# Kernel tuning notes

Hardware: AMD Instinct MI355X
Metric: run time of the kernel (lower is better)

The kernel has to match this reference:

```python
import jax, jax.numpy as jnp
import numpy as np

N_EVENTS = 16
N_SAMPLES = 2 ** 15          # 32768
STEP = 256                   # window_size // 2
LONG_WINDOW = 4096
LONG_COEFFS = LONG_WINDOW // 2 + 1   # 2049
LONG_STEP = LONG_WINDOW // 2         # 2048
LONG_FRAMES = N_SAMPLES // LONG_STEP # 16
N_FRAMES = N_SAMPLES // STEP         # 128
B = 8                                 # audio batch
BE = B * N_EVENTS                     # event batch = 128


def setup_inputs() -> dict:
    key = jax.random.key(0)
    k1, k2, k3, k4 = jax.random.split(key, 4)
    env = jax.random.uniform(k1, (BE, LONG_WINDOW, LONG_FRAMES), jnp.float32)
    tf = jax.random.normal(k2, (BE, LONG_COEFFS * 2, LONG_FRAMES), jnp.float32)
    noise = jax.random.uniform(k3, (BE, LONG_WINDOW, LONG_FRAMES), jnp.float32)
    indices = jax.random.randint(k4, (B, N_EVENTS), 0, N_FRAMES, dtype=jnp.int32)
    return {"env": env, "tf": tf, "noise": noise, "indices": indices}


def _event_render(env, tf, noise):
    # env, noise: (BE, LONG_WINDOW, LONG_FRAMES); tf: (BE, 2*LONG_COEFFS, LONG_FRAMES)
    batch = env.shape[0]
    energy = env * (noise * 2.0 - 1.0)  # uniform_(-1, 1) noise scaled by amp

    # magnitude = norm over interleaved (real, imag) pairs, per torch view semantics
    pairs = tf.reshape(batch, LONG_COEFFS, 2, LONG_FRAMES)
    mag = jnp.sqrt(jnp.sum(pairs * pairs, axis=2))  # (batch, C, F)
    mx = jnp.max(mag.reshape(batch, -1), axis=-1, keepdims=True)
    mag = (mag.reshape(batch, -1) / (mx + 1e-8)).reshape(batch, LONG_COEFFS, LONG_FRAMES)
    imag = tf[:, LONG_COEFFS:, :]
    phase = jnp.arctan2(imag, mag) * np.pi  # torch.angle(complex(mag, imag)) * pi
    tfc = mag * jnp.exp(1j * phase)         # complex transfer fn (batch, C, F)

    # sequential per-frame recurrence: state feeds through rfft/irfft filtering
    e_t = jnp.transpose(energy, (2, 0, 1))  # (F, batch, W)
    t_t = jnp.transpose(tfc, (2, 0, 1))     # (F, batch, C)

    def step(prev, inp):
        e, t = inp
        local = prev + e
        spec = jnp.fft.rfft(local, axis=-1, norm='ortho') * t
        frame = jnp.fft.irfft(spec, n=LONG_WINDOW, axis=-1, norm='ortho')
        return frame, frame

    init = jnp.zeros((batch, LONG_WINDOW), energy.dtype)
    _, frames = jax.lax.scan(step, init, (e_t, t_t))   # (F, batch, W)
    frames = jnp.transpose(frames, (1, 0, 2))          # (batch, F, W)

    # overlap-add with hop = LONG_STEP = W/2: split frames into halves and add
    halves = frames.reshape(batch, LONG_FRAMES, 2, LONG_STEP)
    out = jnp.zeros((batch, LONG_FRAMES + 1, LONG_STEP), frames.dtype)
    out = out.at[:, :LONG_FRAMES].add(halves[:, :, 0])
    out = out.at[:, 1:].add(halves[:, :, 1])
    return out.reshape(batch, -1)[:, :N_SAMPLES]       # (BE, N_SAMPLES)


def _segment_render(atoms, indices):
    # atoms: (BE, N_SAMPLES) -> (B, N_EVENTS, N_SAMPLES); scatter-add at time offsets
    x = atoms.reshape(B, N_EVENTS, N_SAMPLES)
    times = indices * STEP                                      # (B, E)
    pos = times[:, :, None] + jnp.arange(N_SAMPLES)[None, None, :]  # (B, E, S)
    out = jnp.zeros((B, 2 * N_SAMPLES), x.dtype)
    bidx = jnp.arange(B)[:, None, None]
    out = out.at[bidx, pos].add(x)
    return out[:, None, :N_SAMPLES]                             # (B, 1, N_SAMPLES)


def reference(env, tf, noise, indices):
    atoms = _event_render(env, tf, noise)
    return _segment_render(atoms, indices)
```

## Files before the change

### kernel.cpp

```cpp
#include <hip/hip_runtime.h>
#include <math.h>

#define TWO_PI 6.283185307179586f

#define OFF_ET   0ull
#define OFF_E    8388608ull
#define OFF_MAXP 16781312ull
#define OFF_Z    16782336ull

__device__ __forceinline__ int sw2(int n) { return n ^ ((n >> 4) & 15); }

__device__ __forceinline__ int permf(int k) {
    return ((k & 1) << 10) | (((k >> 1) & 3) << 8) | (((k >> 3) & 3) << 6)
         | (((k >> 5) & 3) << 4) | (((k >> 7) & 3) << 2) | ((k >> 9) & 3);
}

__device__ __forceinline__ void r4f_core(float2* b, int p0, int p1, int p2, int p3,
                                         float c1, float s1, float c2, float s2, float c3, float s3) {
    float2 A = b[p0], Bv = b[p1], C = b[p2], D = b[p3];
    float u0r = A.x + C.x, u0i = A.y + C.y;
    float u1r = A.x - C.x, u1i = A.y - C.y;
    float u2r = Bv.x + D.x, u2i = Bv.y + D.y;
    float u3r = Bv.x - D.x, u3i = Bv.y - D.y;
    b[p0] = make_float2(u0r + u2r, u0i + u2i);
    float z1r = u1r + u3i, z1i = u1i - u3r;
    b[p1] = make_float2(z1r * c1 + z1i * s1, z1i * c1 - z1r * s1);
    float z2r = u0r - u2r, z2i = u0i - u2i;
    b[p2] = make_float2(z2r * c2 + z2i * s2, z2i * c2 - z2r * s2);
    float z3r = u1r - u3i, z3i = u1i + u3r;
    b[p3] = make_float2(z3r * c3 + z3i * s3, z3i * c3 - z3r * s3);
}

__device__ __forceinline__ void r4i_core(float2* b, int p0, int p1, int p2, int p3,
                                         float c1, float s1, float c2, float s2, float c3, float s3) {
    float2 z0 = b[p0], z1 = b[p1], z2 = b[p2], z3 = b[p3];
    float t1r = z1.x * c1 - z1.y * s1, t1i = z1.y * c1 + z1.x * s1;
    float t2r = z2.x * c2 - z2.y * s2, t2i = z2.y * c2 + z2.x * s2;
    float t3r = z3.x * c3 - z3.y * s3, t3i = z3.y * c3 + z3.x * s3;
    float u0r = z0.x + t2r, u0i = z0.y + t2i;
    float u1r = z0.x - t2r, u1i = z0.y - t2i;
    float u2r = t1r + t3r, u2i = t1i + t3i;
    float u3r = t1r - t3r, u3i = t1i - t3i;
    b[p0] = make_float2(u0r + u2r, u0i + u2i);
    b[p1] = make_float2(u1r - u3i, u1i + u3r);
    b[p2] = make_float2(u0r - u2r, u0i - u2i);
    b[p3] = make_float2(u1r + u3i, u1i - u3r);
}

#define STAGE4X(CORE, JEXPR, H, ANGEXPR)                                       \
    {                                                                          \
        _Pragma("unroll")                                                      \
        for (int half_ = 0; half_ < 2; ++half_) {                              \
            int b_ = tid + half_ * 1024;                                       \
            int i_ = b_ & 511;                                                 \
            float2* bb_ = B2 + (b_ >> 9) * 2048;                               \
            int j_ = (JEXPR);                                                  \
            int p0 = sw2(j_), p1 = sw2(j_ + (H)), p2 = sw2(j_ + 2 * (H)),      \
                p3 = sw2(j_ + 3 * (H));                                        \
            float s1, c1; __sincosf((ANGEXPR), &s1, &c1);                      \
            float c2 = c1 * c1 - s1 * s1, s2 = 2.f * c1 * s1;                  \
            float c3 = c1 * c2 - s1 * s2, s3 = s1 * c2 + c1 * s2;              \
            CORE(bb_, p0, p1, p2, p3, c1, s1, c2, s2, c3, s3);                 \
        }                                                                      \
    }                                                                          \
    __syncthreads();

__global__ __launch_bounds__(1024, 8) void k_fwd(const float* __restrict__ env,
                                                 const float* __restrict__ noise,
                                                 const float* __restrict__ tf,
                                                 float* __restrict__ ws) {
    __shared__ float2 B2[8192];
    int tid = threadIdx.x;
    int id = blockIdx.x;
    int xcd = id & 7, slot = id >> 3;
    int be = xcd * 16 + (slot >> 2);
    int fg = slot & 3;
    const float4* env4 = (const float4*)env;
    const float4* noi4 = (const float4*)noise;
    size_t base = (size_t)be * 16384 + fg;

#pragma unroll
    for (int it = 0; it < 2; ++it) {
        int c = tid + it * 1024;
        float4 ea = env4[base + (size_t)(2 * c) * 4];
        float4 eb = env4[base + (size_t)(2 * c + 1) * 4];
        float4 za = noi4[base + (size_t)(2 * c) * 4];
        float4 zb = noi4[base + (size_t)(2 * c + 1) * 4];
        int m = sw2(c);
        B2[m]        = make_float2(ea.x * (za.x * 2.f - 1.f), eb.x * (zb.x * 2.f - 1.f));
        B2[2048 + m] = make_float2(ea.y * (za.y * 2.f - 1.f), eb.y * (zb.y * 2.f - 1.f));
        B2[4096 + m] = make_float2(ea.z * (za.z * 2.f - 1.f), eb.z * (zb.z * 2.f - 1.f));
        B2[6144 + m] = make_float2(ea.w * (za.w * 2.f - 1.f), eb.w * (zb.w * 2.f - 1.f));
    }
    __syncthreads();
    {
        int i = tid;
        int sj = sw2(i), sjb = sw2(i + 1024);
        float s, c; __sincosf((float)i * (TWO_PI / 2048.0f), &s, &c);
#pragma unroll
        for (int j4 = 0; j4 < 4; ++j4) {
            float2* bb = B2 + j4 * 2048;
            float2 a = bb[sj], b = bb[sjb];
            float dr = a.x - b.x, di = a.y - b.y;
            bb[sj] = make_float2(a.x + b.x, a.y + b.y);
            bb[sjb] = make_float2(dr * c + di * s, di * c - dr * s);
        }
    }
    __syncthreads();
    STAGE4X(r4f_core, (i_ >> 8) * 1024 + (i_ & 255), 256, (float)(i_ & 255) * (TWO_PI / 1024.0f));
    STAGE4X(r4f_core, (i_ >> 6) * 256 + (i_ & 63), 64, (float)(i_ & 63) * (TWO_PI / 256.0f));
    STAGE4X(r4f_core, (i_ >> 4) * 64 + (i_ & 15), 16, (float)(i_ & 15) * (TWO_PI / 64.0f));
    STAGE4X(r4f_core, (i_ >> 2) * 16 + (i_ & 3), 4, (float)(i_ & 3) * (TWO_PI / 16.0f));
    STAGE4X(r4f_core, i_ * 4, 1, 0.0f);
    float2* Ebase = (float2*)(ws + OFF_E) + (size_t)(be * 16 + fg * 4) * 2049;
    for (int k = tid; k <= 1024; k += 1024) {
        int pk = sw2(permf(k));
        int pm = sw2(permf((2048 - k) & 2047));
        float s4, c4; __sincosf((float)k * (TWO_PI / 4096.0f), &s4, &c4);
#pragma unroll
        for (int j4 = 0; j4 < 4; ++j4) {
            float2* bb = B2 + j4 * 2048;
            float2 zk = bb[pk], zm = bb[pm];
            float xer = 0.5f * (zk.x + zm.x), xei = 0.5f * (zk.y - zm.y);
            float xor_ = 0.5f * (zk.y + zm.y), xoi = 0.5f * (zm.x - zk.x);
            float wr = xor_ * c4 + xoi * s4;
            float wi = xoi * c4 - xor_ * s4;
            float2* Eg = Ebase + (size_t)j4 * 2049;
            Eg[k] = make_float2(xer + wr, xei + wi);
            Eg[2048 - k] = make_float2(xer - wr, wi - xei);
        }
    }
    __syncthreads();
    float* Bf = (float*)B2;
    const float4* ab4 = (const float4*)(tf + (size_t)be * 65568);
    int b0 = fg * 513;
    int nb = (fg == 3) ? 510 : 513;
    float mx = 0.f;
    for (int u = tid; u < nb * 4; u += 1024) {
        int g = u >> 2, e = u & 3;
        int bin = b0 + g;
        float4 A = ab4[bin * 8 + e];
        float4 Bv = ab4[bin * 8 + e + 4];
        mx = fmaxf(mx, fmaxf(fmaxf(A.x * A.x + Bv.x * Bv.x, A.y * A.y + Bv.y * Bv.y),
                             fmaxf(A.z * A.z + Bv.z * Bv.z, A.w * A.w + Bv.w * Bv.w)));
    }
    Bf[tid] = mx;
    __syncthreads();
    for (int s = 512; s > 0; s >>= 1) {
        if (tid < s) Bf[tid] = fmaxf(Bf[tid], Bf[tid + s]);
        __syncthreads();
    }
    if (tid == 0) ws[OFF_MAXP + be * 4 + fg] = Bf[0];
}

__global__ __launch_bounds__(256) void k_recur(const float* __restrict__ tf,
                                               float* __restrict__ ws) {
    __shared__ float sm2lo[256 * 17], simlo[256 * 17];
    __shared__ float sm2hi[256 * 17], simhi[256 * 17];
    int tid = threadIdx.x;
    int be = blockIdx.y;
    int k0 = blockIdx.x << 8;
    int hi0 = 1793 - k0;
    const float* tfb = tf + (size_t)be * 65568;
    const float4* ab4 = (const float4*)tfb;
    const float4* im4 = (const float4*)(tfb + 32784);

    for (int u = tid; u < 2048; u += 256) {
        int half = u >> 10, v = u & 1023;
        int g = v >> 2, e = v & 3;
        int bin = half ? (hi0 + g) : (k0 + g);
        float4 A = ab4[bin * 8 + e];
        float4 Bv = ab4[bin * 8 + e + 4];
        float4 I = im4[bin * 4 + e];
        int o = g * 17 + e * 4;
        float* sm = half ? sm2hi : sm2lo;
        float* si = half ? simhi : simlo;
        sm[o + 0] = A.x * A.x + Bv.x * Bv.x;
        sm[o + 1] = A.y * A.y + Bv.y * Bv.y;
        sm[o + 2] = A.z * A.z + Bv.z * Bv.z;
        sm[o + 3] = A.w * A.w + Bv.w * Bv.w;
        si[o + 0] = I.x; si[o + 1] = I.y; si[o + 2] = I.z; si[o + 3] = I.w;
    }
    __syncthreads();

    int k = k0 + tid;
    int m = 2048 - k;
    int rhi = 255 - tid;
    const float* mp = ws + OFF_MAXP + be * 4;
    float m2x = fmaxf(fmaxf(mp[0], mp[1]), fmaxf(mp[2], mp[3]));
    float rden = 1.0f / (sqrtf(m2x) + 1e-8f);
    const float2* Eb = (const float2*)(ws + OFF_E) + (size_t)be * 16 * 2049;
    float2* Zb = (float2*)(ws + OFF_Z) + (size_t)be * 16 * 2048;
    float2 evlo[16], evhi[16];
#pragma unroll
    for (int f = 0; f < 16; ++f) {
        evlo[f] = Eb[(size_t)f * 2049 + k];
        evhi[f] = Eb[(size_t)f * 2049 + m];
    }
    float ym = (k == 0) ? 0.0f : 1.0f;
    float s4, c4; __sincosf((float)k * (TWO_PI / 4096.0f), &s4, &c4);
    const float SCL = 1.0f / 2048.0f;
    float srl = 0.f, sil = 0.f, srh = 0.f, sih = 0.f;
#pragma unroll
    for (int f = 0; f < 16; ++f) {
        float mh = sqrtf(sm2lo[tid * 17 + f]) * rden;
        float ph = atan2f(simlo[tid * 17 + f], mh) * 3.14159265358979f;
        float sp, cp; __sincosf(ph, &sp, &cp);
        float Tr = mh * cp, Ti = mh * sp;
        sil *= ym;
        srl += evlo[f].x; sil += evlo[f].y;
        float nr = srl * Tr - sil * Ti;
        sil = srl * Ti + sil * Tr; srl = nr;
        float mh2 = sqrtf(sm2hi[rhi * 17 + f]) * rden;
        float ph2 = atan2f(simhi[rhi * 17 + f], mh2) * 3.14159265358979f;
        float sp2, cp2; __sincosf(ph2, &sp2, &cp2);
        float Tr2 = mh2 * cp2, Ti2 = mh2 * sp2;
        sih *= ym;
        srh += evhi[f].x; sih += evhi[f].y;
        float nr2 = srh * Tr2 - sih * Ti2;
        sih = srh * Ti2 + sih * Tr2; srh = nr2;
        float2* Zf = Zb + (size_t)f * 2048;
        if (k == 0) {
            float y0 = srl * SCL, yn = srh * SCL;
            Zf[0] = make_float2(0.5f * (y0 + yn), 0.5f * (y0 - yn));
        } else {
            float ykr = srl * SCL, yki = sil * SCL;
            float ymr = srh * SCL, ymi = sih * SCL;
            float er = 0.5f * (ykr + ymr), ei = 0.5f * (yki - ymi);
            float dr = ykr - ymr, di = yki + ymi;
            float orr = 0.5f * (dr * c4 - di * s4);
            float oi = 0.5f * (dr * s4 + di * c4);
            Zf[k] = make_float2(er - oi, ei + orr);
            Zf[m] = make_float2(er + oi, orr - ei);
        }
    }
    if (k0 == 0 && tid == 0) {
        float sr = 0.f, si = 0.f;
#pragma unroll
        for (int f = 0; f < 16; ++f) {
            float a = tfb[1024 * 32 + f];
            float b = tfb[1024 * 32 + 16 + f];
            float im = tfb[32784 + 1024 * 16 + f];
            float mh = sqrtf(a * a + b * b) * rden;
            float ph = atan2f(im, mh) * 3.14159265358979f;
            float sp, cp; __sincosf(ph, &sp, &cp);
            float Tr = mh * cp, Ti = mh * sp;
            float2 e = Eb[(size_t)f * 2049 + 1024];
            sr += e.x; si += e.y;
            float nr = sr * Tr - si * Ti;
            si = sr * Ti + si * Tr; sr = nr;
            Zb[(size_t)f * 2048 + 1024] = make_float2(sr * SCL, -si * SCL);
        }
    }
}

__global__ __launch_bounds__(1024, 8) void k_fft_inv(float* __restrict__ ws) {
    __shared__ float2 B2[8192];
    int tid = threadIdx.x;
    int be = blockIdx.x >> 2, fg = blockIdx.x & 3;
    const float2* Zbase = (const float2*)(ws + OFF_Z) + (size_t)(be * 16 + fg * 4) * 2048;
    float4 v[4];
#pragma unroll
    for (int j4 = 0; j4 < 4; ++j4)
        v[j4] = ((const float4*)(Zbase + (size_t)j4 * 2048))[tid];
    {
        int n0 = tid * 2;
        int p0 = sw2(permf(n0)), p1 = sw2(permf(n0 + 1));
#pragma unroll
        for (int j4 = 0; j4 < 4; ++j4) {
            float2* bb = B2 + j4 * 2048;
            bb[p0] = make_float2(v[j4].x, v[j4].y);
            bb[p1] = make_float2(v[j4].z, v[j4].w);
        }
    }
    __syncthreads();
    STAGE4X(r4i_core, i_ * 4, 1, 0.0f);
    STAGE4X(r4i_core, (i_ >> 2) * 16 + (i_ & 3), 4, (float)(i_ & 3) * (TWO_PI / 16.0f));
    STAGE4X(r4i_core, (i_ >> 4) * 64 + (i_ & 15), 16, (float)(i_ & 15) * (TWO_PI / 64.0f));
    STAGE4X(r4i_core, (i_ >> 6) * 256 + (i_ & 63), 64, (float)(i_ & 63) * (TWO_PI / 256.0f));
    STAGE4X(r4i_core, (i_ >> 8) * 1024 + (i_ & 255), 256, (float)(i_ & 255) * (TWO_PI / 1024.0f));
    {
        int i = tid;
        int sj = sw2(i), sjb = sw2(i + 1024);
        float s, c; __sincosf((float)i * (TWO_PI / 2048.0f), &s, &c);
#pragma unroll
        for (int j4 = 0; j4 < 4; ++j4) {
            float2* bb = B2 + j4 * 2048;
            float2 b = bb[sjb];
            float tr = b.x * c - b.y * s, ti2 = b.x * s + b.y * c;
            float2 a = bb[sj];
            bb[sj] = make_float2(a.x + tr, a.y + ti2);
            bb[sjb] = make_float2(a.x - tr, a.y - ti2);
        }
    }
    __syncthreads();
    float2* Fbase = (float2*)(ws + OFF_ET) + (size_t)(be * 16 + fg * 4) * 2048;
#pragma unroll
    for (int j4 = 0; j4 < 4; ++j4) {
        float2* bb = B2 + j4 * 2048;
        float2* Fg = Fbase + (size_t)j4 * 2048;
#pragma unroll
        for (int it = 0; it < 2; ++it) {
            int m = tid + it * 1024;
            Fg[m] = bb[sw2(m)];
        }
    }
}

__global__ __launch_bounds__(256) void k_segment(const float* __restrict__ ws,
                                                 const int* __restrict__ indices,
                                                 float* __restrict__ out) {
    __shared__ int ste[16];
    int tid = threadIdx.x;
    int b = blockIdx.y;
    if (tid < 16) ste[tid] = indices[b * 16 + tid] * 256;
    __syncthreads();
    int g = blockIdx.x * 256 + tid;
    int t = g << 2;
    const float* F = ws + OFF_ET;
    float4 acc = make_float4(0.f, 0.f, 0.f, 0.f);
#pragma unroll
    for (int e = 0; e < 16; ++e) {
        int te = ste[e];
        if (t >= te) {
            int d = t - te;
            int j = d >> 11, r = d & 2047;
            size_t base = (size_t)(b * 16 + e) * 65536;
            float4 v = *(const float4*)(F + base + j * 4096 + r);
            acc.x += v.x; acc.y += v.y; acc.z += v.z; acc.w += v.w;
            if (j >= 1) {
                float4 w = *(const float4*)(F + base + (j - 1) * 4096 + 2048 + r);
                acc.x += w.x; acc.y += w.y; acc.z += w.z; acc.w += w.w;
            }
        }
    }
    ((float4*)out)[(size_t)b * 8192 + g] = acc;
}

extern "C" void kernel_launch(void* const* d_in, const int* in_sizes, int n_in,
                              void* d_out, int out_size, void* d_ws, size_t ws_size,
                              hipStream_t stream) {
    const float* env = (const float*)d_in[0];
    const float* tf = (const float*)d_in[1];
    const float* noise = (const float*)d_in[2];
    const int* indices = (const int*)d_in[3];
    float* ws = (float*)d_ws;
    float* out = (float*)d_out;

    k_fwd<<<dim3(512), dim3(1024), 0, stream>>>(env, noise, tf, ws);
    k_recur<<<dim3(4, 128), dim3(256), 0, stream>>>(tf, ws);
    k_fft_inv<<<dim3(512), dim3(1024), 0, stream>>>(ws);
    k_segment<<<dim3(32, 8), dim3(256), 0, stream>>>(ws, indices, out);
}
```

Baseline: 88.72 us.

## Replace radix-2/4 FFT stages with radix-8 passes and fewer barriers

Rewrites the 2048-point complex FFTs in the forward and inverse kernels as three radix-8 stages plus one radix-4 stage, in place of one radix-2 and five radix-4 stages. Each group of 256 threads now owns one of the four buffers, and a new 5-bit XOR swizzle with a matching digit-reversal permutation replaces the old ones. The goal is fewer shared-memory passes and __syncthreads barriers, plus fewer twiddle sincos calls. In exchange each thread holds more registers, and twiddles are built by repeated complex multiplication, which may cost some accuracy.

```diff
diff --git a/kernel.cpp b/kernel.cpp
--- a/kernel.cpp
+++ b/kernel.cpp
@@ -8,62 +8,103 @@
 #define OFF_MAXP 16781312ull
 #define OFF_Z    16782336ull
 
-__device__ __forceinline__ int sw2(int n) { return n ^ ((n >> 4) & 15); }
-
-__device__ __forceinline__ int permf(int k) {
-    return ((k & 1) << 10) | (((k >> 1) & 3) << 8) | (((k >> 3) & 3) << 6)
-         | (((k >> 5) & 3) << 4) | (((k >> 7) & 3) << 2) | ((k >> 9) & 3);
-}
-
-__device__ __forceinline__ void r4f_core(float2* b, int p0, int p1, int p2, int p3,
-                                         float c1, float s1, float c2, float s2, float c3, float s3) {
-    float2 A = b[p0], Bv = b[p1], C = b[p2], D = b[p3];
-    float u0r = A.x + C.x, u0i = A.y + C.y;
-    float u1r = A.x - C.x, u1i = A.y - C.y;
-    float u2r = Bv.x + D.x, u2i = Bv.y + D.y;
-    float u3r = Bv.x - D.x, u3i = Bv.y - D.y;
-    b[p0] = make_float2(u0r + u2r, u0i + u2i);
-    float z1r = u1r + u3i, z1i = u1i - u3r;
-    b[p1] = make_float2(z1r * c1 + z1i * s1, z1i * c1 - z1r * s1);
-    float z2r = u0r - u2r, z2i = u0i - u2i;
-    b[p2] = make_float2(z2r * c2 + z2i * s2, z2i * c2 - z2r * s2);
-    float z3r = u1r - u3i, z3i = u1i + u3r;
-    b[p3] = make_float2(z3r * c3 + z3i * s3, z3i * c3 - z3r * s3);
-}
-
-__device__ __forceinline__ void r4i_core(float2* b, int p0, int p1, int p2, int p3,
-                                         float c1, float s1, float c2, float s2, float c3, float s3) {
-    float2 z0 = b[p0], z1 = b[p1], z2 = b[p2], z3 = b[p3];
-    float t1r = z1.x * c1 - z1.y * s1, t1i = z1.y * c1 + z1.x * s1;
-    float t2r = z2.x * c2 - z2.y * s2, t2i = z2.y * c2 + z2.x * s2;
-    float t3r = z3.x * c3 - z3.y * s3, t3i = z3.y * c3 + z3.x * s3;
-    float u0r = z0.x + t2r, u0i = z0.y + t2i;
-    float u1r = z0.x - t2r, u1i = z0.y - t2i;
-    float u2r = t1r + t3r, u2i = t1i + t3i;
-    float u3r = t1r - t3r, u3i = t1i - t3i;
-    b[p0] = make_float2(u0r + u2r, u0i + u2i);
-    b[p1] = make_float2(u1r - u3i, u1i + u3r);
-    b[p2] = make_float2(u0r - u2r, u0i - u2i);
-    b[p3] = make_float2(u1r + u3i, u1i - u3r);
-}
-
-#define STAGE4X(CORE, JEXPR, H, ANGEXPR)                                       \
-    {                                                                          \
-        _Pragma("unroll")                                                      \
-        for (int half_ = 0; half_ < 2; ++half_) {                              \
-            int b_ = tid + half_ * 1024;                                       \
-            int i_ = b_ & 511;                                                 \
-            float2* bb_ = B2 + (b_ >> 9) * 2048;                               \
-            int j_ = (JEXPR);                                                  \
-            int p0 = sw2(j_), p1 = sw2(j_ + (H)), p2 = sw2(j_ + 2 * (H)),      \
-                p3 = sw2(j_ + 3 * (H));                                        \
-            float s1, c1; __sincosf((ANGEXPR), &s1, &c1);                      \
-            float c2 = c1 * c1 - s1 * s1, s2 = 2.f * c1 * s1;                  \
-            float c3 = c1 * c2 - s1 * s2, s3 = s1 * c2 + c1 * s2;              \
-            CORE(bb_, p0, p1, p2, p3, c1, s1, c2, s2, c3, s3);                 \
-        }                                                                      \
-    }                                                                          \
-    __syncthreads();
+__device__ __forceinline__ int sw(int i) { return i ^ ((i >> 5) & 31); }
+
+__device__ __forceinline__ int posf(int k) {
+    return ((k & 7) << 8) | (((k >> 3) & 7) << 5) | (((k >> 6) & 7) << 2) | (k >> 9);
+}
+
+__device__ __forceinline__ float2 cmul(float2 a, float2 b) {
+    return make_float2(a.x * b.x - a.y * b.y, a.x * b.y + a.y * b.x);
+}
+__device__ __forceinline__ float2 cadd(float2 a, float2 b) { return make_float2(a.x + b.x, a.y + b.y); }
+__device__ __forceinline__ float2 csub(float2 a, float2 b) { return make_float2(a.x - b.x, a.y - b.y); }
+
+#define RH 0.70710678118654752f
+
+__device__ __forceinline__ void r8f(float2* b, int i0, int stride, float theta) {
+    float2 x0 = b[sw(i0)],            x1 = b[sw(i0 + stride)];
+    float2 x2 = b[sw(i0 + 2*stride)], x3 = b[sw(i0 + 3*stride)];
+    float2 x4 = b[sw(i0 + 4*stride)], x5 = b[sw(i0 + 5*stride)];
+    float2 x6 = b[sw(i0 + 6*stride)], x7 = b[sw(i0 + 7*stride)];
+    float2 t0 = cadd(x0, x4), t1 = csub(x0, x4), t2 = cadd(x2, x6), t3 = csub(x2, x6);
+    float2 A0 = cadd(t0, t2), A2 = csub(t0, t2);
+    float2 A1 = make_float2(t1.x + t3.y, t1.y - t3.x);
+    float2 A3 = make_float2(t1.x - t3.y, t1.y + t3.x);
+    float2 u0 = cadd(x1, x5), u1 = csub(x1, x5), u2 = cadd(x3, x7), u3 = csub(x3, x7);
+    float2 B0 = cadd(u0, u2), B2 = csub(u0, u2);
+    float2 B1 = make_float2(u1.x + u3.y, u1.y - u3.x);
+    float2 B3 = make_float2(u1.x - u3.y, u1.y + u3.x);
+    float2 b1 = make_float2((B1.x + B1.y) * RH, (B1.y - B1.x) * RH);
+    float2 b2 = make_float2(B2.y, -B2.x);
+    float2 b3 = make_float2((B3.y - B3.x) * RH, -(B3.x + B3.y) * RH);
+    float2 y0 = cadd(A0, B0), y4 = csub(A0, B0);
+    float2 y1 = cadd(A1, b1), y5 = csub(A1, b1);
+    float2 y2 = cadd(A2, b2), y6 = csub(A2, b2);
+    float2 y3 = cadd(A3, b3), y7 = csub(A3, b3);
+    float s1, c1; __sincosf(theta, &s1, &c1);
+    float2 w1 = make_float2(c1, -s1), w = w1;
+    y1 = cmul(y1, w); w = cmul(w, w1);
+    y2 = cmul(y2, w); w = cmul(w, w1);
+    y3 = cmul(y3, w); w = cmul(w, w1);
+    y4 = cmul(y4, w); w = cmul(w, w1);
+    y5 = cmul(y5, w); w = cmul(w, w1);
+    y6 = cmul(y6, w); w = cmul(w, w1);
+    y7 = cmul(y7, w);
+    b[sw(i0)]            = y0; b[sw(i0 + stride)]   = y1;
+    b[sw(i0 + 2*stride)] = y2; b[sw(i0 + 3*stride)] = y3;
+    b[sw(i0 + 4*stride)] = y4; b[sw(i0 + 5*stride)] = y5;
+    b[sw(i0 + 6*stride)] = y6; b[sw(i0 + 7*stride)] = y7;
+}
+
+__device__ __forceinline__ void r4f(float2* b, int i0) {
+    float2 a0 = b[sw(i0)], a1 = b[sw(i0 + 1)], a2 = b[sw(i0 + 2)], a3 = b[sw(i0 + 3)];
+    float2 t0 = cadd(a0, a2), t1 = csub(a0, a2), t2 = cadd(a1, a3), t3 = csub(a1, a3);
+    b[sw(i0)]     = cadd(t0, t2);
+    b[sw(i0 + 1)] = make_float2(t1.x + t3.y, t1.y - t3.x);
+    b[sw(i0 + 2)] = csub(t0, t2);
+    b[sw(i0 + 3)] = make_float2(t1.x - t3.y, t1.y + t3.x);
+}
+
+__device__ __forceinline__ void r8i(float2* b, int i0, int stride, float theta) {
+    float2 z0 = b[sw(i0)],            z1 = b[sw(i0 + stride)];
+    float2 z2 = b[sw(i0 + 2*stride)], z3 = b[sw(i0 + 3*stride)];
+    float2 z4 = b[sw(i0 + 4*stride)], z5 = b[sw(i0 + 5*stride)];
+    float2 z6 = b[sw(i0 + 6*stride)], z7 = b[sw(i0 + 7*stride)];
+    float s1, c1; __sincosf(theta, &s1, &c1);
+    float2 w1 = make_float2(c1, s1), w = w1;
+    z1 = cmul(z1, w); w = cmul(w, w1);
+    z2 = cmul(z2, w); w = cmul(w, w1);
+    z3 = cmul(z3, w); w = cmul(w, w1);
+    z4 = cmul(z4, w); w = cmul(w, w1);
+    z5 = cmul(z5, w); w = cmul(w, w1);
+    z6 = cmul(z6, w); w = cmul(w, w1);
+    z7 = cmul(z7, w);
+    float2 t0 = cadd(z0, z4), t1 = csub(z0, z4), t2 = cadd(z2, z6), t3 = csub(z2, z6);
+    float2 A0 = cadd(t0, t2), A2 = csub(t0, t2);
+    float2 A1 = make_float2(t1.x - t3.y, t1.y + t3.x);
+    float2 A3 = make_float2(t1.x + t3.y, t1.y - t3.x);
+    float2 u0 = cadd(z1, z5), u1 = csub(z1, z5), u2 = cadd(z3, z7), u3 = csub(z3, z7);
+    float2 B0 = cadd(u0, u2), B2 = csub(u0, u2);
+    float2 B1 = make_float2(u1.x - u3.y, u1.y + u3.x);
+    float2 B3 = make_float2(u1.x + u3.y, u1.y - u3.x);
+    float2 b1 = make_float2((B1.x - B1.y) * RH, (B1.x + B1.y) * RH);
+    float2 b2 = make_float2(-B2.y, B2.x);
+    float2 b3 = make_float2(-(B3.x + B3.y) * RH, (B3.x - B3.y) * RH);
+    b[sw(i0)]            = cadd(A0, B0); b[sw(i0 + 4*stride)] = csub(A0, B0);
+    b[sw(i0 + stride)]   = cadd(A1, b1); b[sw(i0 + 5*stride)] = csub(A1, b1);
+    b[sw(i0 + 2*stride)] = cadd(A2, b2); b[sw(i0 + 6*stride)] = csub(A2, b2);
+    b[sw(i0 + 3*stride)] = cadd(A3, b3); b[sw(i0 + 7*stride)] = csub(A3, b3);
+}
+
+__device__ __forceinline__ void r4i(float2* b, int i0) {
+    float2 a0 = b[sw(i0)], a1 = b[sw(i0 + 1)], a2 = b[sw(i0 + 2)], a3 = b[sw(i0 + 3)];
+    float2 t0 = cadd(a0, a2), t1 = csub(a0, a2), t2 = cadd(a1, a3), t3 = csub(a1, a3);
+    b[sw(i0)]     = cadd(t0, t2);
+    b[sw(i0 + 1)] = make_float2(t1.x - t3.y, t1.y + t3.x);
+    b[sw(i0 + 2)] = csub(t0, t2);
+    b[sw(i0 + 3)] = make_float2(t1.x + t3.y, t1.y - t3.x);
+}
 
 __global__ __launch_bounds__(1024, 8) void k_fwd(const float* __restrict__ env,
                                                  const float* __restrict__ noise,
@@ -78,7 +119,6 @@
     const float4* env4 = (const float4*)env;
     const float4* noi4 = (const float4*)noise;
     size_t base = (size_t)be * 16384 + fg;
-
 #pragma unroll
     for (int it = 0; it < 2; ++it) {
         int c = tid + it * 1024;
@@ -86,46 +126,36 @@
         float4 eb = env4[base + (size_t)(2 * c + 1) * 4];
         float4 za = noi4[base + (size_t)(2 * c) * 4];
         float4 zb = noi4[base + (size_t)(2 * c + 1) * 4];
-        int m = sw2(c);
+        int m = sw(c);
         B2[m]        = make_float2(ea.x * (za.x * 2.f - 1.f), eb.x * (zb.x * 2.f - 1.f));
         B2[2048 + m] = make_float2(ea.y * (za.y * 2.f - 1.f), eb.y * (zb.y * 2.f - 1.f));
         B2[4096 + m] = make_float2(ea.z * (za.z * 2.f - 1.f), eb.z * (zb.z * 2.f - 1.f));
         B2[6144 + m] = make_float2(ea.w * (za.w * 2.f - 1.f), eb.w * (zb.w * 2.f - 1.f));
     }
     __syncthreads();
-    {
-        int i = tid;
-        int sj = sw2(i), sjb = sw2(i + 1024);
-        float s, c; __sincosf((float)i * (TWO_PI / 2048.0f), &s, &c);
-#pragma unroll
-        for (int j4 = 0; j4 < 4; ++j4) {
-            float2* bb = B2 + j4 * 2048;
-            float2 a = bb[sj], b = bb[sjb];
-            float dr = a.x - b.x, di = a.y - b.y;
-            bb[sj] = make_float2(a.x + b.x, a.y + b.y);
-            bb[sjb] = make_float2(dr * c + di * s, di * c - dr * s);
-        }
-    }
-    __syncthreads();
-    STAGE4X(r4f_core, (i_ >> 8) * 1024 + (i_ & 255), 256, (float)(i_ & 255) * (TWO_PI / 1024.0f));
-    STAGE4X(r4f_core, (i_ >> 6) * 256 + (i_ & 63), 64, (float)(i_ & 63) * (TWO_PI / 256.0f));
-    STAGE4X(r4f_core, (i_ >> 4) * 64 + (i_ & 15), 16, (float)(i_ & 15) * (TWO_PI / 64.0f));
-    STAGE4X(r4f_core, (i_ >> 2) * 16 + (i_ & 3), 4, (float)(i_ & 3) * (TWO_PI / 16.0f));
-    STAGE4X(r4f_core, i_ * 4, 1, 0.0f);
-    float2* Ebase = (float2*)(ws + OFF_E) + (size_t)(be * 16 + fg * 4) * 2049;
-    for (int k = tid; k <= 1024; k += 1024) {
-        int pk = sw2(permf(k));
-        int pm = sw2(permf((2048 - k) & 2047));
-        float s4, c4; __sincosf((float)k * (TWO_PI / 4096.0f), &s4, &c4);
-#pragma unroll
-        for (int j4 = 0; j4 < 4; ++j4) {
-            float2* bb = B2 + j4 * 2048;
+    int buf = tid >> 8, t = tid & 255;
+    float2* bb = B2 + buf * 2048;
+    r8f(bb, t, 256, (float)t * (TWO_PI / 2048.f));
+    __syncthreads();
+    r8f(bb, (t >> 5) * 256 + (t & 31), 32, (float)(t & 31) * (TWO_PI / 256.f));
+    __syncthreads();
+    r8f(bb, (t >> 2) * 32 + (t & 3), 4, (float)(t & 3) * (TWO_PI / 32.f));
+    __syncthreads();
+    r4f(bb, 8 * t); r4f(bb, 8 * t + 4);
+    __syncthreads();
+    float2* Eg = (float2*)(ws + OFF_E) + (size_t)(be * 16 + fg * 4 + buf) * 2049;
+#pragma unroll
+    for (int it = 0; it < 5; ++it) {
+        int k = t + it * 256;
+        if (k <= 1024) {
+            int pk = sw(posf(k));
+            int pm = sw(posf((2048 - k) & 2047));
+            float s4, c4; __sincosf((float)k * (TWO_PI / 4096.f), &s4, &c4);
             float2 zk = bb[pk], zm = bb[pm];
             float xer = 0.5f * (zk.x + zm.x), xei = 0.5f * (zk.y - zm.y);
-            float xor_ = 0.5f * (zk.y + zm.y), xoi = 0.5f * (zm.x - zk.x);
-            float wr = xor_ * c4 + xoi * s4;
-            float wi = xoi * c4 - xor_ * s4;
-            float2* Eg = Ebase + (size_t)j4 * 2049;
+            float xo_r = 0.5f * (zk.y + zm.y), xo_i = 0.5f * (zm.x - zk.x);
+            float wr = xo_r * c4 + xo_i * s4;
+            float wi = xo_i * c4 - xo_r * s4;
             Eg[k] = make_float2(xer + wr, xei + wi);
             Eg[2048 - k] = make_float2(xer - wr, wi - xei);
         }
@@ -258,52 +288,31 @@
     __shared__ float2 B2[8192];
     int tid = threadIdx.x;
     int be = blockIdx.x >> 2, fg = blockIdx.x & 3;
-    const float2* Zbase = (const float2*)(ws + OFF_Z) + (size_t)(be * 16 + fg * 4) * 2048;
-    float4 v[4];
-#pragma unroll
-    for (int j4 = 0; j4 < 4; ++j4)
-        v[j4] = ((const float4*)(Zbase + (size_t)j4 * 2048))[tid];
-    {
-        int n0 = tid * 2;
-        int p0 = sw2(permf(n0)), p1 = sw2(permf(n0 + 1));
-#pragma unroll
-        for (int j4 = 0; j4 < 4; ++j4) {
-            float2* bb = B2 + j4 * 2048;
-            bb[p0] = make_float2(v[j4].x, v[j4].y);
-            bb[p1] = make_float2(v[j4].z, v[j4].w);
-        }
-    }
-    __syncthreads();
-    STAGE4X(r4i_core, i_ * 4, 1, 0.0f);
-    STAGE4X(r4i_core, (i_ >> 2) * 16 + (i_ & 3), 4, (float)(i_ & 3) * (TWO_PI / 16.0f));
-    STAGE4X(r4i_core, (i_ >> 4) * 64 + (i_ & 15), 16, (float)(i_ & 15) * (TWO_PI / 64.0f));
-    STAGE4X(r4i_core, (i_ >> 6) * 256 + (i_ & 63), 64, (float)(i_ & 63) * (TWO_PI / 256.0f));
-    STAGE4X(r4i_core, (i_ >> 8) * 1024 + (i_ & 255), 256, (float)(i_ & 255) * (TWO_PI / 1024.0f));
-    {
-        int i = tid;
-        int sj = sw2(i), sjb = sw2(i + 1024);
-        float s, c; __sincosf((float)i * (TWO_PI / 2048.0f), &s, &c);
-#pragma unroll
-        for (int j4 = 0; j4 < 4; ++j4) {
-            float2* bb = B2 + j4 * 2048;
-            float2 b = bb[sjb];
-            float tr = b.x * c - b.y * s, ti2 = b.x * s + b.y * c;
-            float2 a = bb[sj];
-            bb[sj] = make_float2(a.x + tr, a.y + ti2);
-            bb[sjb] = make_float2(a.x - tr, a.y - ti2);
-        }
-    }
-    __syncthreads();
-    float2* Fbase = (float2*)(ws + OFF_ET) + (size_t)(be * 16 + fg * 4) * 2048;
-#pragma unroll
-    for (int j4 = 0; j4 < 4; ++j4) {
-        float2* bb = B2 + j4 * 2048;
-        float2* Fg = Fbase + (size_t)j4 * 2048;
-#pragma unroll
-        for (int it = 0; it < 2; ++it) {
-            int m = tid + it * 1024;
-            Fg[m] = bb[sw2(m)];
-        }
+    int buf = tid >> 8, t = tid & 255;
+    float2* bb = B2 + buf * 2048;
+    const float4* Z4 = (const float4*)((float2*)(ws + OFF_Z) + (size_t)(be * 16 + fg * 4 + buf) * 2048);
+#pragma unroll
+    for (int it = 0; it < 4; ++it) {
+        int idx = t + it * 256;
+        float4 v = Z4[idx];
+        int k0 = idx * 2;
+        bb[sw(posf(k0))]     = make_float2(v.x, v.y);
+        bb[sw(posf(k0 + 1))] = make_float2(v.z, v.w);
+    }
+    __syncthreads();
+    r4i(bb, 8 * t); r4i(bb, 8 * t + 4);
+    __syncthreads();
+    r8i(bb, (t >> 2) * 32 + (t & 3), 4, (float)(t & 3) * (TWO_PI / 32.f));
+    __syncthreads();
+    r8i(bb, (t >> 5) * 256 + (t & 31), 32, (float)(t & 31) * (TWO_PI / 256.f));
+    __syncthreads();
+    r8i(bb, t, 256, (float)t * (TWO_PI / 2048.f));
+    __syncthreads();
+    float2* Fg = (float2*)(ws + OFF_ET) + (size_t)(be * 16 + fg * 4 + buf) * 2048;
+#pragma unroll
+    for (int it = 0; it < 8; ++it) {
+        int c = t + it * 256;
+        Fg[c] = bb[sw(c)];
     }
 }
 
```

Result: slower. 92.54 us (+4.3%).
